# Kernel tuning notes

Hardware: AMD Instinct MI355X
Metric: run time of the kernel (lower is better)

The kernel has to match this reference:

```python
import jax, jax.numpy as jnp
import numpy as np

NEG_BIG = -9e15
ALPHA = 0.2  # leaky relu slope

def setup_inputs() -> dict:
    key = jax.random.key(0)
    k1, k2, k3, k4, k5 = jax.random.split(key, 5)
    N, F_in, F_out, H = 4096, 512, 64, 8
    x = jax.random.normal(k1, (N, F_in), dtype=jnp.float32)
    adj = jax.random.randint(k2, (N, N), 0, 2, dtype=jnp.int32)
    W = jax.random.normal(k3, (H, F_in, F_out), dtype=jnp.float32) * (1.414 * (2.0 / (F_in + F_out)) ** 0.5)
    a_source = jax.random.normal(k4, (H, 1, F_out), dtype=jnp.float32) * (1.414 * (2.0 / (1 + F_out)) ** 0.5)
    a_target = jax.random.normal(k5, (H, 1, F_out), dtype=jnp.float32) * (1.414 * (2.0 / (1 + F_out)) ** 0.5)
    return {"x": x, "adj": adj, "W": W, "a_source": a_source, "a_target": a_target}

def reference(x, adj, W, a_source, a_target):
    # Wh: [H, N, F_out]
    Wh = jnp.einsum('nf,hfo->hno', x, W)
    # additive attention logits
    s_i = jnp.sum(a_source * Wh, axis=2, keepdims=True)          # [H, N, 1]
    s_j = jnp.sum(a_target * Wh, axis=2, keepdims=True)          # [H, N, 1]
    e = s_i + jnp.swapaxes(s_j, 1, 2)                            # [H, N, N]
    e = jnp.where(e > 0, e, ALPHA * e)                           # leaky relu
    e = jnp.where(adj[None] > 0, e, jnp.float32(NEG_BIG))        # adjacency mask
    attention = jax.nn.softmax(e, axis=2)                        # [H, N, N]
    h_prime = jnp.einsum('hij,hjo->hio', attention, Wh)          # [H, N, F_out]
    return h_prime
```

## Files before the change

### kernel.cpp

```cpp
#include <hip/hip_runtime.h>
#include <hip/hip_fp16.h>
#include <cstdint>

#define N_NODES 4096
#define F_IN    512
#define F_OUT   64
#define H_HEADS 8
#define JC      4

constexpr float L2E = 1.44269504088896f;

typedef _Float16 half2_t __attribute__((ext_vector_type(2)));
typedef _Float16 half4_t __attribute__((ext_vector_type(4)));
typedef _Float16 half8_t __attribute__((ext_vector_type(8)));
typedef float    f32x4   __attribute__((ext_vector_type(4)));

__device__ inline unsigned int exp2_pk_u(unsigned int au) {
    __half2 h = __builtin_bit_cast(__half2, au);
    h = h2exp2(h);
    return __builtin_bit_cast(unsigned int, h);
}

__global__ __launch_bounds__(256) void k_prep(const int* __restrict__ adj,
                                              const float* __restrict__ W,
                                              unsigned long long* __restrict__ adjwT,
                                              _Float16* __restrict__ wfrag) {
    if (blockIdx.x < 128) {
        int gid = blockIdx.x * 256 + threadIdx.x;
        int h     = gid >> 12;
        int kt    = (gid >> 8) & 15;
        int ntile = (gid >> 6) & 3;
        int lane  = gid & 63;
        int c0 = lane & 15, g = lane >> 4;
        const float* src = W + ((size_t)h * F_IN + kt * 32 + 8 * g) * F_OUT + ntile * 16 + c0;
        half8_t hv;
        #pragma unroll
        for (int t = 0; t < 8; t++) hv[t] = (_Float16)src[(size_t)t * F_OUT];
        *reinterpret_cast<half8_t*>(&wfrag[(size_t)gid * 8]) = hv;
        return;
    }
    int bid  = blockIdx.x - 128;
    int lane = threadIdx.x & 63;
    int wid  = (int)((bid * 256 + threadIdx.x) >> 6);
    int nwaves = (2048 * 256) >> 6;
    const int nchunks = N_NODES * (N_NODES / 64);
    for (int cf = wid; cf < nchunks; cf += nwaves) {
        int v = adj[(size_t)cf * 64 + lane];
        unsigned long long mask = __ballot(v > 0);
        if (lane == 0) {
            int i = cf >> 6, c = cf & 63;
            adjwT[(size_t)c * N_NODES + i] = mask;
        }
    }
}

__global__ __launch_bounds__(512) void k_wh_mfma(const float* __restrict__ x,
                                                 const _Float16* __restrict__ wfrag,
                                                 const float* __restrict__ a_src,
                                                 const float* __restrict__ a_tgt,
                                                 _Float16* __restrict__ WhFrag,
                                                 float* __restrict__ s_iL,
                                                 _Float16* __restrict__ s_jLh) {
    __shared__ _Float16 xs[16 * 512];
    const int rt   = blockIdx.x;
    const int t    = threadIdx.x;
    const int lane = t & 63;
    const int h    = t >> 6;
    const int c0   = lane & 15;
    const int gl   = lane >> 4;

    {
        const int srow = t >> 5;
        const int seg  = t & 31;
        const float* src = x + (size_t)(rt * 16 + srow) * F_IN + seg * 16;
        _Float16* drow = &xs[srow * 512];
        #pragma unroll
        for (int j = 0; j < 2; j++) {
            float4 v0 = *reinterpret_cast<const float4*>(src + j * 8);
            float4 v1 = *reinterpret_cast<const float4*>(src + j * 8 + 4);
            half8_t hv;
            hv[0] = (_Float16)v0.x; hv[1] = (_Float16)v0.y; hv[2] = (_Float16)v0.z; hv[3] = (_Float16)v0.w;
            hv[4] = (_Float16)v1.x; hv[5] = (_Float16)v1.y; hv[6] = (_Float16)v1.z; hv[7] = (_Float16)v1.w;
            int u  = seg * 2 + j;
            int up = u ^ (srow & 7);
            *reinterpret_cast<half8_t*>(&drow[up * 8]) = hv;
        }
    }
    __syncthreads();

    f32x4 acc0 = {0.f, 0.f, 0.f, 0.f};
    f32x4 acc1 = {0.f, 0.f, 0.f, 0.f};
    f32x4 acc2 = {0.f, 0.f, 0.f, 0.f};
    f32x4 acc3 = {0.f, 0.f, 0.f, 0.f};

    const _Float16* __restrict__ Bf   = wfrag + (size_t)h * (16 * 4 * 512) + (size_t)lane * 8;
    const _Float16* __restrict__ arow = &xs[c0 * 512];

    #pragma unroll
    for (int kt = 0; kt < 16; kt++) {
        int up = (kt * 4 + gl) ^ (c0 & 7);
        half8_t a = *reinterpret_cast<const half8_t*>(&arow[up * 8]);
        const _Float16* Bk = Bf + (size_t)kt * 2048;
        half8_t b0 = *reinterpret_cast<const half8_t*>(Bk);
        half8_t b1 = *reinterpret_cast<const half8_t*>(Bk + 512);
        half8_t b2 = *reinterpret_cast<const half8_t*>(Bk + 1024);
        half8_t b3 = *reinterpret_cast<const half8_t*>(Bk + 1536);
        acc0 = __builtin_amdgcn_mfma_f32_16x16x32_f16(a, b0, acc0, 0, 0, 0);
        acc1 = __builtin_amdgcn_mfma_f32_16x16x32_f16(a, b1, acc1, 0, 0, 0);
        acc2 = __builtin_amdgcn_mfma_f32_16x16x32_f16(a, b2, acc2, 0, 0, 0);
        acc3 = __builtin_amdgcn_mfma_f32_16x16x32_f16(a, b3, acc3, 0, 0, 0);
    }

    const float as0 = a_src[h * 64 + c0],      at0 = a_tgt[h * 64 + c0];
    const float as1 = a_src[h * 64 + 16 + c0], at1 = a_tgt[h * 64 + 16 + c0];
    const float as2 = a_src[h * 64 + 32 + c0], at2 = a_tgt[h * 64 + 32 + c0];
    const float as3 = a_src[h * 64 + 48 + c0], at3 = a_tgt[h * 64 + 48 + c0];

    #pragma unroll
    for (int reg = 0; reg < 4; reg++) {
        float vi = acc0[reg] * as0 + acc1[reg] * as1 + acc2[reg] * as2 + acc3[reg] * as3;
        float vj = acc0[reg] * at0 + acc1[reg] * at1 + acc2[reg] * at2 + acc3[reg] * at3;
        #pragma unroll
        for (int mm = 8; mm >= 1; mm >>= 1) {
            vi += __shfl_xor(vi, mm, 64);
            vj += __shfl_xor(vj, mm, 64);
        }
        if (c0 == 0) {
            int row = rt * 16 + 4 * gl + reg;
            s_iL[h * N_NODES + row]  = vi * L2E;
            s_jLh[h * N_NODES + row] = (_Float16)(vj * L2E);
        }
    }

    const int cc    = rt >> 2;
    const int kb    = (rt >> 1) & 1;
    const int lanep = c0 + 16 * ((rt & 1) * 2 + (gl >> 1));
    const int tb    = 4 * (gl & 1);
    _Float16* dst = WhFrag + (size_t)h * (N_NODES * 64)
                  + (size_t)(cc * 2 + kb) * 2048 + (size_t)lanep * 8 + tb;
    f32x4 accs[4] = {acc0, acc1, acc2, acc3};
    #pragma unroll
    for (int ot = 0; ot < 4; ot++) {
        half4_t hv;
        #pragma unroll
        for (int reg = 0; reg < 4; reg++) hv[reg] = (_Float16)accs[ot][reg];
        *reinterpret_cast<half4_t*>(dst + ot * 512) = hv;
    }
}

__global__ __launch_bounds__(256) void k_hmax(const _Float16* __restrict__ s_jLh,
                                              float* __restrict__ mxAll) {
    __shared__ float red[4];
    const int h = blockIdx.x;
    const int t = threadIdx.x;
    const _Float16* p = s_jLh + h * N_NODES;
    float m = -INFINITY;
    for (int k = t; k < N_NODES; k += 256) m = fmaxf(m, (float)p[k]);
    #pragma unroll
    for (int mm = 32; mm >= 1; mm >>= 1) m = fmaxf(m, __shfl_xor(m, mm, 64));
    if ((t & 63) == 0) red[t >> 6] = m;
    __syncthreads();
    if (t == 0) mxAll[h] = fmaxf(fmaxf(red[0], red[1]), fmaxf(red[2], red[3]));
}

__global__ __launch_bounds__(256, 4) void k_attn_mfma(const _Float16* __restrict__ WhFrag,
                                                      const float* __restrict__ s_iL,
                                                      const float* __restrict__ mxAll,
                                                      const _Float16* __restrict__ s_jLh,
                                                      const unsigned long long* __restrict__ adjwT,
                                                      float* __restrict__ out0,
                                                      _Float16* __restrict__ partH,
                                                      float* __restrict__ lbuf) {
    __shared__ uint2 ktab4[16];
    __shared__ _Float16 Bs[2][4096];
    if (threadIdx.x < 16) {
        unsigned int nib = threadIdx.x;
        unsigned int w0 = ((nib & 1u) ? 0xFFFFu : 0u) | ((nib & 2u) ? 0xFFFF0000u : 0u);
        unsigned int w1 = ((nib & 4u) ? 0xFFFFu : 0u) | ((nib & 8u) ? 0xFFFF0000u : 0u);
        ktab4[nib] = make_uint2(w0, w1);
    }

    const int tid  = threadIdx.x;
    const int h    = blockIdx.y;
    const int jc   = blockIdx.z;
    const int lane = tid & 63;
    const int w    = tid >> 6;
    const int i0   = blockIdx.x * 128 + w * 32;
    const int mrow = lane & 15;
    const int gl   = lane >> 4;
    const int gl8  = gl << 3;

    const float siL0 = s_iL[h * N_NODES + i0 + mrow];
    const float siL1 = s_iL[h * N_NODES + i0 + 16 + mrow];
    const float mxh  = mxAll[h];
    const float tm0 = siL0 + mxh, tm1 = siL1 + mxh;
    const float m0 = fmaxf(tm0, 0.2f * tm0);
    const float m1 = fmaxf(tm1, 0.2f * tm1);
    const half2_t u2_0 = {(_Float16)(siL0 - m0), (_Float16)(siL0 - m0)};
    const half2_t u2_1 = {(_Float16)(siL1 - m1), (_Float16)(siL1 - m1)};
    const half2_t n82_0 = {(_Float16)(-0.8f * m0), (_Float16)(-0.8f * m0)};
    const half2_t n82_1 = {(_Float16)(-0.8f * m1), (_Float16)(-0.8f * m1)};
    const half2_t c02 = {(_Float16)0.2f, (_Float16)0.2f};

    const _Float16* __restrict__ sjh = s_jLh + h * N_NODES;
    const _Float16* __restrict__ Bh  = WhFrag + (size_t)h * (N_NODES * 64);

    half8_t vone;
    #pragma unroll
    for (int q = 0; q < 8; q++) vone[q] = (_Float16)1.0f;

    f32x4 accA0 = {0,0,0,0}, accA1 = {0,0,0,0}, accA2 = {0,0,0,0}, accA3 = {0,0,0,0};
    f32x4 accB0 = {0,0,0,0}, accB1 = {0,0,0,0}, accB2 = {0,0,0,0}, accB3 = {0,0,0,0};
    f32x4 acclA = {0,0,0,0}, acclB = {0,0,0,0};

    const int NC   = (N_NODES / 64) / JC;
    const int cbeg = jc * NC;
    const int cend = cbeg + NC;

    {
        const _Float16* src = Bh + (size_t)cbeg * 4096 + tid * 8;
        *reinterpret_cast<half8_t*>(&Bs[0][tid * 8])        = *reinterpret_cast<const half8_t*>(src);
        *reinterpret_cast<half8_t*>(&Bs[0][2048 + tid * 8]) = *reinterpret_cast<const half8_t*>(src + 2048);
    }
    __syncthreads();

    int cur = 0;
    for (int c = cbeg; c < cend; c++) {
        half8_t n0, n1;
        const bool hasNext = (c + 1 < cend);
        if (hasNext) {
            const _Float16* src = Bh + (size_t)(c + 1) * 4096 + tid * 8;
            n0 = *reinterpret_cast<const half8_t*>(src);
            n1 = *reinterpret_cast<const half8_t*>(src + 2048);
        }

        uint2 word0 = *reinterpret_cast<const uint2*>(&adjwT[(size_t)c * N_NODES + i0 + mrow]);
        uint2 word1 = *reinterpret_cast<const uint2*>(&adjwT[(size_t)c * N_NODES + i0 + 16 + mrow]);

        #pragma unroll
        for (int kb = 0; kb < 2; kb++) {
            const int jb = c * 64 + kb * 32 + 8 * gl;
            half8_t sjv = *reinterpret_cast<const half8_t*>(&sjh[jb]);
            unsigned int bm0 = ((kb ? word0.y : word0.x) >> gl8) & 0xFFu;
            unsigned int bm1 = ((kb ? word1.y : word1.x) >> gl8) & 0xFFu;
            uint2 klo0 = ktab4[bm0 & 15u], khi0 = ktab4[bm0 >> 4];
            uint2 klo1 = ktab4[bm1 & 15u], khi1 = ktab4[bm1 >> 4];
            uint4 mk0 = {klo0.x, klo0.y, khi0.x, khi0.y};
            uint4 mk1 = {klo1.x, klo1.y, khi1.x, khi1.y};

            uint4 sju = __builtin_bit_cast(uint4, sjv);
            uint4 p0u, p1u;
            #pragma unroll
            for (int q = 0; q < 4; q++) {
                unsigned int sw = (q == 0) ? sju.x : (q == 1) ? sju.y : (q == 2) ? sju.z : sju.w;
                half2_t sj2 = __builtin_bit_cast(half2_t, sw);
                half2_t a1 = u2_0 + sj2;
                half2_t am = __builtin_elementwise_max(a1, a1 * c02 + n82_0);
                unsigned int pa = exp2_pk_u(__builtin_bit_cast(unsigned int, am));
                half2_t b1 = u2_1 + sj2;
                half2_t bmv = __builtin_elementwise_max(b1, b1 * c02 + n82_1);
                unsigned int pb = exp2_pk_u(__builtin_bit_cast(unsigned int, bmv));
                unsigned int ka  = (q == 0) ? mk0.x : (q == 1) ? mk0.y : (q == 2) ? mk0.z : mk0.w;
                unsigned int kbm = (q == 0) ? mk1.x : (q == 1) ? mk1.y : (q == 2) ? mk1.z : mk1.w;
                pa &= ka; pb &= kbm;
                if (q == 0) { p0u.x = pa; p1u.x = pb; }
                else if (q == 1) { p0u.y = pa; p1u.y = pb; }
                else if (q == 2) { p0u.z = pa; p1u.z = pb; }
                else { p0u.w = pa; p1u.w = pb; }
            }
            half8_t af0 = __builtin_bit_cast(half8_t, p0u);
            half8_t af1 = __builtin_bit_cast(half8_t, p1u);

            const _Float16* Bk = &Bs[cur][kb * 2048 + lane * 8];
            half8_t b0  = *reinterpret_cast<const half8_t*>(Bk);
            half8_t b1v = *reinterpret_cast<const half8_t*>(Bk + 512);
            half8_t b2  = *reinterpret_cast<const half8_t*>(Bk + 1024);
            half8_t b3  = *reinterpret_cast<const half8_t*>(Bk + 1536);

            accA0 = __builtin_amdgcn_mfma_f32_16x16x32_f16(af0, b0,  accA0, 0, 0, 0);
            accB0 = __builtin_amdgcn_mfma_f32_16x16x32_f16(af1, b0,  accB0, 0, 0, 0);
            accA1 = __builtin_amdgcn_mfma_f32_16x16x32_f16(af0, b1v, accA1, 0, 0, 0);
            accB1 = __builtin_amdgcn_mfma_f32_16x16x32_f16(af1, b1v, accB1, 0, 0, 0);
            accA2 = __builtin_amdgcn_mfma_f32_16x16x32_f16(af0, b2,  accA2, 0, 0, 0);
            accB2 = __builtin_amdgcn_mfma_f32_16x16x32_f16(af1, b2,  accB2, 0, 0, 0);
            accA3 = __builtin_amdgcn_mfma_f32_16x16x32_f16(af0, b3,  accA3, 0, 0, 0);
            accB3 = __builtin_amdgcn_mfma_f32_16x16x32_f16(af1, b3,  accB3, 0, 0, 0);
            acclA = __builtin_amdgcn_mfma_f32_16x16x32_f16(af0, vone, acclA, 0, 0, 0);
            acclB = __builtin_amdgcn_mfma_f32_16x16x32_f16(af1, vone, acclB, 0, 0, 0);
        }

        if (hasNext) {
            *reinterpret_cast<half8_t*>(&Bs[cur ^ 1][tid * 8])        = n0;
            *reinterpret_cast<half8_t*>(&Bs[cur ^ 1][2048 + tid * 8]) = n1;
        }
        __syncthreads();
        cur ^= 1;
    }

    float* lp = lbuf + (size_t)jc * (H_HEADS * N_NODES);
    if (mrow == 0) {
        #pragma unroll
        for (int r = 0; r < 4; r++) {
            lp[h * N_NODES + i0 + 4 * gl + r]      = acclA[r];
            lp[h * N_NODES + i0 + 16 + 4 * gl + r] = acclB[r];
        }
    }
    if (jc == 0) {
        #pragma unroll
        for (int r = 0; r < 4; r++) {
            size_t obA = ((size_t)h * N_NODES + i0 + 4 * gl + r) * 64 + mrow;
            size_t obB = ((size_t)h * N_NODES + i0 + 16 + 4 * gl + r) * 64 + mrow;
            out0[obA + 0]  = accA0[r];
            out0[obA + 16] = accA1[r];
            out0[obA + 32] = accA2[r];
            out0[obA + 48] = accA3[r];
            out0[obB + 0]  = accB0[r];
            out0[obB + 16] = accB1[r];
            out0[obB + 32] = accB2[r];
            out0[obB + 48] = accB3[r];
        }
    } else {
        _Float16* op = partH + (size_t)(jc - 1) * ((size_t)H_HEADS * N_NODES * F_OUT);
        #pragma unroll
        for (int r = 0; r < 4; r++) {
            size_t obA = ((size_t)h * N_NODES + i0 + 4 * gl + r) * 64 + mrow;
            size_t obB = ((size_t)h * N_NODES + i0 + 16 + 4 * gl + r) * 64 + mrow;
            op[obA + 0]  = (_Float16)accA0[r];
            op[obA + 16] = (_Float16)accA1[r];
            op[obA + 32] = (_Float16)accA2[r];
            op[obA + 48] = (_Float16)accA3[r];
            op[obB + 0]  = (_Float16)accB0[r];
            op[obB + 16] = (_Float16)accB1[r];
            op[obB + 32] = (_Float16)accB2[r];
            op[obB + 48] = (_Float16)accB3[r];
        }
    }
}

__global__ __launch_bounds__(256) void k_norm(float* __restrict__ out,
                                              const _Float16* __restrict__ partH,
                                              const float* __restrict__ lbuf) {
    const int HN = H_HEADS * N_NODES;
    int idx = blockIdx.x * 256 + threadIdx.x;
    int row = idx >> 4;
    float inv = 1.0f / (lbuf[row] + lbuf[HN + row] + lbuf[2 * HN + row] + lbuf[3 * HN + row]);
    float4 a = reinterpret_cast<const float4*>(out)[idx];
    float s0 = a.x, s1 = a.y, s2 = a.z, s3 = a.w;
    #pragma unroll
    for (int p = 0; p < 3; p++) {
        half4_t hp = *reinterpret_cast<const half4_t*>(
            &partH[(size_t)p * ((size_t)H_HEADS * N_NODES * F_OUT) + (size_t)idx * 4]);
        s0 += (float)hp[0]; s1 += (float)hp[1]; s2 += (float)hp[2]; s3 += (float)hp[3];
    }
    float4 v = {s0 * inv, s1 * inv, s2 * inv, s3 * inv};
    reinterpret_cast<float4*>(out)[idx] = v;
}

extern "C" void kernel_launch(void* const* d_in, const int* in_sizes, int n_in,
                              void* d_out, int out_size, void* d_ws, size_t ws_size,
                              hipStream_t stream) {
    const float* x     = (const float*)d_in[0];
    const int*   adj   = (const int*)d_in[1];
    const float* W     = (const float*)d_in[2];
    const float* a_src = (const float*)d_in[3];
    const float* a_tgt = (const float*)d_in[4];
    float* out = (float*)d_out;

    char* ws = (char*)d_ws;
    size_t off = 0;
    auto alloc = [&](size_t bytes) -> char* {
        char* p = ws + off;
        off += (bytes + 255) & ~(size_t)255;
        return p;
    };
    _Float16* WhFrag = (_Float16*)alloc((size_t)H_HEADS * N_NODES * F_OUT * 2);
    _Float16* wfrag  = (_Float16*)alloc((size_t)H_HEADS * 16 * 4 * 64 * 8 * 2);
    float* s_iL      = (float*)alloc((size_t)H_HEADS * N_NODES * 4);
    _Float16* s_jLh  = (_Float16*)alloc((size_t)H_HEADS * N_NODES * 2);
    float* mxAll     = (float*)alloc((size_t)H_HEADS * 4);
    float* lbuf      = (float*)alloc((size_t)JC * H_HEADS * N_NODES * 4);
    _Float16* partH  = (_Float16*)alloc((size_t)(JC - 1) * H_HEADS * N_NODES * F_OUT * 2);
    unsigned long long* adjwT = (unsigned long long*)alloc((size_t)N_NODES * (N_NODES / 64) * 8);
    (void)ws_size;

    k_prep<<<2176, 256, 0, stream>>>(adj, W, adjwT, wfrag);
    k_wh_mfma<<<N_NODES / 16, 512, 0, stream>>>(x, wfrag, a_src, a_tgt, WhFrag, s_iL, s_jLh);
    k_hmax<<<H_HEADS, 256, 0, stream>>>(s_jLh, mxAll);
    k_attn_mfma<<<dim3(N_NODES / 128, H_HEADS, JC), 256, 0, stream>>>(WhFrag, s_iL, mxAll, s_jLh,
                                                                      adjwT, out, partH, lbuf);
    k_norm<<<(H_HEADS * N_NODES * F_OUT / 4) / 256, 256, 0, stream>>>(out, partH, lbuf);
}
```

Before: 77.06 us.

## Factor exp2 of leaky-relu logits into per-row and per-column exponential products

Since exp2 is monotone, exp2(leakyrelu(s_i+s_j)-m) equals the max of two products: one of per-row and per-column exponentials for the positive branch, and one for the 0.2-slope branch. The per-column factors F1=exp2(s_j-mx) and F2=exp2(0.2*(s_j-mx)) are now precomputed in the max-reduction kernel, which also switches s_j storage to fp32. The attention inner loop then uses two packed multiplies and a max instead of add, fma, max and a packed exp2. This removes transcendental work from the hot loop but doubles the per-column fp16 loads, and the fp16 products may lose precision or underflow for large logit spreads.

```diff
diff --git a/kernel.cpp b/kernel.cpp
--- a/kernel.cpp
+++ b/kernel.cpp
@@ -14,12 +14,6 @@
 typedef _Float16 half4_t __attribute__((ext_vector_type(4)));
 typedef _Float16 half8_t __attribute__((ext_vector_type(8)));
 typedef float    f32x4   __attribute__((ext_vector_type(4)));
-
-__device__ inline unsigned int exp2_pk_u(unsigned int au) {
-    __half2 h = __builtin_bit_cast(__half2, au);
-    h = h2exp2(h);
-    return __builtin_bit_cast(unsigned int, h);
-}
 
 __global__ __launch_bounds__(256) void k_prep(const int* __restrict__ adj,
                                               const float* __restrict__ W,
@@ -60,7 +54,7 @@
                                                  const float* __restrict__ a_tgt,
                                                  _Float16* __restrict__ WhFrag,
                                                  float* __restrict__ s_iL,
-                                                 _Float16* __restrict__ s_jLh) {
+                                                 float* __restrict__ s_jL) {
     __shared__ _Float16 xs[16 * 512];
     const int rt   = blockIdx.x;
     const int t    = threadIdx.x;
@@ -127,8 +121,8 @@
         }
         if (c0 == 0) {
             int row = rt * 16 + 4 * gl + reg;
-            s_iL[h * N_NODES + row]  = vi * L2E;
-            s_jLh[h * N_NODES + row] = (_Float16)(vj * L2E);
+            s_iL[h * N_NODES + row] = vi * L2E;
+            s_jL[h * N_NODES + row] = vj * L2E;
         }
     }
 
@@ -148,25 +142,46 @@
     }
 }
 
-__global__ __launch_bounds__(256) void k_hmax(const _Float16* __restrict__ s_jLh,
-                                              float* __restrict__ mxAll) {
+__global__ __launch_bounds__(256) void k_hmax(const float* __restrict__ s_jL,
+                                              float* __restrict__ mxAll,
+                                              _Float16* __restrict__ F1h,
+                                              _Float16* __restrict__ F2h) {
     __shared__ float red[4];
+    __shared__ float mxs;
     const int h = blockIdx.x;
     const int t = threadIdx.x;
-    const _Float16* p = s_jLh + h * N_NODES;
+    const float* p = s_jL + h * N_NODES;
+    float v[16];
     float m = -INFINITY;
-    for (int k = t; k < N_NODES; k += 256) m = fmaxf(m, (float)p[k]);
+    #pragma unroll
+    for (int i = 0; i < 16; i++) {
+        v[i] = p[t + i * 256];
+        m = fmaxf(m, v[i]);
+    }
     #pragma unroll
     for (int mm = 32; mm >= 1; mm >>= 1) m = fmaxf(m, __shfl_xor(m, mm, 64));
     if ((t & 63) == 0) red[t >> 6] = m;
     __syncthreads();
-    if (t == 0) mxAll[h] = fmaxf(fmaxf(red[0], red[1]), fmaxf(red[2], red[3]));
+    if (t == 0) {
+        float mx = fmaxf(fmaxf(red[0], red[1]), fmaxf(red[2], red[3]));
+        mxAll[h] = mx;
+        mxs = mx;
+    }
+    __syncthreads();
+    const float mx = mxs;
+    #pragma unroll
+    for (int i = 0; i < 16; i++) {
+        float d = v[i] - mx;
+        F1h[h * N_NODES + t + i * 256] = (_Float16)exp2f(d);
+        F2h[h * N_NODES + t + i * 256] = (_Float16)exp2f(0.2f * d);
+    }
 }
 
 __global__ __launch_bounds__(256, 4) void k_attn_mfma(const _Float16* __restrict__ WhFrag,
                                                       const float* __restrict__ s_iL,
                                                       const float* __restrict__ mxAll,
-                                                      const _Float16* __restrict__ s_jLh,
+                                                      const _Float16* __restrict__ F1h,
+                                                      const _Float16* __restrict__ F2h,
                                                       const unsigned long long* __restrict__ adjwT,
                                                       float* __restrict__ out0,
                                                       _Float16* __restrict__ partH,
@@ -196,14 +211,16 @@
     const float tm0 = siL0 + mxh, tm1 = siL1 + mxh;
     const float m0 = fmaxf(tm0, 0.2f * tm0);
     const float m1 = fmaxf(tm1, 0.2f * tm1);
-    const half2_t u2_0 = {(_Float16)(siL0 - m0), (_Float16)(siL0 - m0)};
-    const half2_t u2_1 = {(_Float16)(siL1 - m1), (_Float16)(siL1 - m1)};
-    const half2_t n82_0 = {(_Float16)(-0.8f * m0), (_Float16)(-0.8f * m0)};
-    const half2_t n82_1 = {(_Float16)(-0.8f * m1), (_Float16)(-0.8f * m1)};
-    const half2_t c02 = {(_Float16)0.2f, (_Float16)0.2f};
-
-    const _Float16* __restrict__ sjh = s_jLh + h * N_NODES;
-    const _Float16* __restrict__ Bh  = WhFrag + (size_t)h * (N_NODES * 64);
+    const _Float16 E1A = (_Float16)exp2f(tm0 - m0);
+    const _Float16 E2A = (_Float16)exp2f(fmaf(0.2f, tm0, -m0));
+    const _Float16 E1B = (_Float16)exp2f(tm1 - m1);
+    const _Float16 E2B = (_Float16)exp2f(fmaf(0.2f, tm1, -m1));
+    const half2_t e1a = {E1A, E1A}, e2a = {E2A, E2A};
+    const half2_t e1b = {E1B, E1B}, e2b = {E2B, E2B};
+
+    const _Float16* __restrict__ F1 = F1h + h * N_NODES;
+    const _Float16* __restrict__ F2 = F2h + h * N_NODES;
+    const _Float16* __restrict__ Bh = WhFrag + (size_t)h * (N_NODES * 64);
 
     half8_t vone;
     #pragma unroll
@@ -240,7 +257,8 @@
         #pragma unroll
         for (int kb = 0; kb < 2; kb++) {
             const int jb = c * 64 + kb * 32 + 8 * gl;
-            half8_t sjv = *reinterpret_cast<const half8_t*>(&sjh[jb]);
+            half8_t f1v = *reinterpret_cast<const half8_t*>(&F1[jb]);
+            half8_t f2v = *reinterpret_cast<const half8_t*>(&F2[jb]);
             unsigned int bm0 = ((kb ? word0.y : word0.x) >> gl8) & 0xFFu;
             unsigned int bm1 = ((kb ? word1.y : word1.x) >> gl8) & 0xFFu;
             uint2 klo0 = ktab4[bm0 & 15u], khi0 = ktab4[bm0 >> 4];
@@ -248,21 +266,21 @@
             uint4 mk0 = {klo0.x, klo0.y, khi0.x, khi0.y};
             uint4 mk1 = {klo1.x, klo1.y, khi1.x, khi1.y};
 
-            uint4 sju = __builtin_bit_cast(uint4, sjv);
+            uint4 f1u = __builtin_bit_cast(uint4, f1v);
+            uint4 f2u = __builtin_bit_cast(uint4, f2v);
             uint4 p0u, p1u;
             #pragma unroll
             for (int q = 0; q < 4; q++) {
-                unsigned int sw = (q == 0) ? sju.x : (q == 1) ? sju.y : (q == 2) ? sju.z : sju.w;
-                half2_t sj2 = __builtin_bit_cast(half2_t, sw);
-                half2_t a1 = u2_0 + sj2;
-                half2_t am = __builtin_elementwise_max(a1, a1 * c02 + n82_0);
-                unsigned int pa = exp2_pk_u(__builtin_bit_cast(unsigned int, am));
-                half2_t b1 = u2_1 + sj2;
-                half2_t bmv = __builtin_elementwise_max(b1, b1 * c02 + n82_1);
-                unsigned int pb = exp2_pk_u(__builtin_bit_cast(unsigned int, bmv));
+                unsigned int f1w = (q == 0) ? f1u.x : (q == 1) ? f1u.y : (q == 2) ? f1u.z : f1u.w;
+                unsigned int f2w = (q == 0) ? f2u.x : (q == 1) ? f2u.y : (q == 2) ? f2u.z : f2u.w;
+                half2_t f12 = __builtin_bit_cast(half2_t, f1w);
+                half2_t f22 = __builtin_bit_cast(half2_t, f2w);
+                half2_t pA = __builtin_elementwise_max(e1a * f12, e2a * f22);
+                half2_t pB = __builtin_elementwise_max(e1b * f12, e2b * f22);
                 unsigned int ka  = (q == 0) ? mk0.x : (q == 1) ? mk0.y : (q == 2) ? mk0.z : mk0.w;
                 unsigned int kbm = (q == 0) ? mk1.x : (q == 1) ? mk1.y : (q == 2) ? mk1.z : mk1.w;
-                pa &= ka; pb &= kbm;
+                unsigned int pa = __builtin_bit_cast(unsigned int, pA) & ka;
+                unsigned int pb = __builtin_bit_cast(unsigned int, pB) & kbm;
                 if (q == 0) { p0u.x = pa; p1u.x = pb; }
                 else if (q == 1) { p0u.y = pa; p1u.y = pb; }
                 else if (q == 2) { p0u.z = pa; p1u.z = pb; }
@@ -376,7 +394,9 @@
     _Float16* WhFrag = (_Float16*)alloc((size_t)H_HEADS * N_NODES * F_OUT * 2);
     _Float16* wfrag  = (_Float16*)alloc((size_t)H_HEADS * 16 * 4 * 64 * 8 * 2);
     float* s_iL      = (float*)alloc((size_t)H_HEADS * N_NODES * 4);
-    _Float16* s_jLh  = (_Float16*)alloc((size_t)H_HEADS * N_NODES * 2);
+    float* s_jL      = (float*)alloc((size_t)H_HEADS * N_NODES * 4);
+    _Float16* F1h    = (_Float16*)alloc((size_t)H_HEADS * N_NODES * 2);
+    _Float16* F2h    = (_Float16*)alloc((size_t)H_HEADS * N_NODES * 2);
     float* mxAll     = (float*)alloc((size_t)H_HEADS * 4);
     float* lbuf      = (float*)alloc((size_t)JC * H_HEADS * N_NODES * 4);
     _Float16* partH  = (_Float16*)alloc((size_t)(JC - 1) * H_HEADS * N_NODES * F_OUT * 2);
@@ -384,9 +404,9 @@
     (void)ws_size;
 
     k_prep<<<2176, 256, 0, stream>>>(adj, W, adjwT, wfrag);
-    k_wh_mfma<<<N_NODES / 16, 512, 0, stream>>>(x, wfrag, a_src, a_tgt, WhFrag, s_iL, s_jLh);
-    k_hmax<<<H_HEADS, 256, 0, stream>>>(s_jLh, mxAll);
-    k_attn_mfma<<<dim3(N_NODES / 128, H_HEADS, JC), 256, 0, stream>>>(WhFrag, s_iL, mxAll, s_jLh,
+    k_wh_mfma<<<N_NODES / 16, 512, 0, stream>>>(x, wfrag, a_src, a_tgt, WhFrag, s_iL, s_jL);
+    k_hmax<<<H_HEADS, 256, 0, stream>>>(s_jL, mxAll, F1h, F2h);
+    k_attn_mfma<<<dim3(N_NODES / 128, H_HEADS, JC), 256, 0, stream>>>(WhFrag, s_iL, mxAll, F1h, F2h,
                                                                       adjwT, out, partH, lbuf);
     k_norm<<<(H_HEADS * N_NODES * F_OUT / 4) / 256, 256, 0, stream>>>(out, partH, lbuf);
 }
```

Result: faster. 68.45 us (median of 2 runs) (-11.2%).
